# Kernel tuning notes

Hardware: AMD Instinct MI355X
Metric: run time of the kernel (lower is better)

Reference implementation:

```python
import jax, jax.numpy as jnp
import numpy as np
import math

B, C, W, H = 8, 512, 32, 32
NUM_HEADS = 4


def setup_inputs() -> dict:
    key = jax.random.key(0)
    ks = jax.random.split(key, 7)
    dqk = C // NUM_HEADS  # out channels of conv_q / conv_k
    s_in = 1.0 / math.sqrt(C)
    return {
        "x": jax.random.normal(ks[0], (B, C, W, H), dtype=jnp.float32),
        "Wq": jax.random.normal(ks[1], (dqk, C), dtype=jnp.float32) * s_in,
        "bq": jnp.zeros((dqk,), dtype=jnp.float32),
        "Wk": jax.random.normal(ks[2], (dqk, C), dtype=jnp.float32) * s_in,
        "bk": jnp.zeros((dqk,), dtype=jnp.float32),
        "Wv": jax.random.normal(ks[3], (C, C), dtype=jnp.float32) * s_in,
        "bv": jnp.zeros((C,), dtype=jnp.float32),
        "gamma": jnp.zeros((1,), dtype=jnp.float32),
    }


def reference(x, Wq, bq, Wk, bk, Wv, bv, gamma):
    b, c, w, h = x.shape
    n = w * h
    heads = NUM_HEADS
    # 1x1 convs == per-pixel linear projections
    q = jnp.einsum('bcwh,oc->bowh', x, Wq) + bq[None, :, None, None]
    k = jnp.einsum('bcwh,oc->bowh', x, Wk) + bk[None, :, None, None]
    v = jnp.einsum('bcwh,oc->bowh', x, Wv) + bv[None, :, None, None]
    # head split exactly as the torch views do
    q = q.reshape(b, heads, (c // heads) // heads, n)  # [B,H,dq,N]
    k = k.reshape(b, heads, (c // heads) // heads, n)  # [B,H,dq,N]
    v = v.reshape(b, heads, c // heads, n)             # [B,H,dv,N]
    scale = math.sqrt(c / heads)  # k_dim = in_dim / num_heads
    scores = jnp.einsum('bhdn,bhdm->bhnm', q, k) / scale  # [B,H,N,N]
    attn = jax.nn.softmax(scores, axis=-1)
    # out = v @ attn^T : out[..., c, n] = sum_m v[..., c, m] * attn[..., n, m]
    out = jnp.einsum('bhcm,bhnm->bhcn', v, attn)  # [B,H,dv,N]
    out = out.reshape(b, c, w, h)
    return gamma * out + x
```

## Files before the change

### kernel.cpp

```cpp
#include <hip/hip_runtime.h>
#include <math.h>

#define BATCH 8
#define CH    512
#define NPIX  1024
#define NH    4

typedef __attribute__((ext_vector_type(8))) short bf16x8;
typedef __attribute__((ext_vector_type(4))) float f32x4;
typedef __attribute__((ext_vector_type(16))) float f32x16;
typedef __attribute__((ext_vector_type(4))) int i32x4;
typedef __attribute__((ext_vector_type(4))) unsigned int u32x4;

#define QSC (0.088388347648318447f * 1.4426950408889634f)

#define GLOAD0(dst, addr) asm volatile("global_load_dwordx4 %0, %1, off" \
    : "=v"(dst) : "v"(addr) : "memory")
#define GLOAD1(dst, addr) asm volatile("global_load_dwordx4 %0, %1, off offset:1024" \
    : "=v"(dst) : "v"(addr) : "memory")
#define WAITV6 asm volatile("s_waitcnt vmcnt(6)" ::: "memory")
#define WAITV0 asm volatile("s_waitcnt vmcnt(0)" ::: "memory")

__device__ inline unsigned short f2bf_rne(float f) {
    unsigned int u = __float_as_uint(f);
    return (unsigned short)((u + 0x7FFFu + ((u >> 16) & 1u)) >> 16);
}
__device__ inline unsigned int pack_bf2_trunc(float a, float b) {
    return (__float_as_uint(a) >> 16) | (__float_as_uint(b) & 0xFFFF0000u);
}
__device__ inline unsigned int pack2_rne(float a, float b) {
    return (unsigned int)f2bf_rne(a) | ((unsigned int)f2bf_rne(b) << 16);
}

__global__ __launch_bounds__(256) void prep(
    const float* __restrict__ x,
    const float* __restrict__ Wq, const float* __restrict__ Wk,
    const float* __restrict__ Wv,
    unsigned short* __restrict__ XTF, unsigned short* __restrict__ WF)
{
    const int t = threadIdx.x;
    if (blockIdx.z == 8) {
        const int gid = blockIdx.y * 16 + blockIdx.x;
        #pragma unroll
        for (int rep = 0; rep < 2; ++rep) {
            const int idx = (rep * 128 + gid) * 256 + t;
            if (idx < 49152) {
                const int o = idx >> 6, k8 = idx & 63;
                const float* src;
                float sc = 1.f;
                if (o < 128)      { src = Wq + (size_t)o * CH;        sc = QSC; }
                else if (o < 256) { src = Wk + (size_t)(o - 128) * CH; }
                else              { src = Wv + (size_t)(o - 256) * CH; }
                src += k8 * 8;
                const float4 v0 = *(const float4*)src;
                const float4 v1 = *(const float4*)(src + 4);
                u32x4 st;
                st.x = pack2_rne(v0.x * sc, v0.y * sc);
                st.y = pack2_rne(v0.z * sc, v0.w * sc);
                st.z = pack2_rne(v1.x * sc, v1.y * sc);
                st.w = pack2_rne(v1.z * sc, v1.w * sc);
                const int dst = (((o >> 4) * 16 + (k8 >> 2)) * 512
                              + (((o & 15) | ((k8 & 3) << 4))) * 8);
                *(u32x4*)&WF[dst] = st;
            }
        }
        return;
    }
    __shared__ float S[64][65];
    const int a = t & 15, g = t >> 4;
    const int n0 = blockIdx.x * 64, c0 = blockIdx.y * 64, b = blockIdx.z;
    const float* xb = x + ((size_t)b * CH + c0) * NPIX + n0;
    #pragma unroll
    for (int i = 0; i < 4; ++i) {
        const int c = g + 16 * i;
        const float4 v = *(const float4*)&xb[(size_t)c * NPIX + 4 * a];
        S[c][4*a+0] = v.x; S[c][4*a+1] = v.y; S[c][4*a+2] = v.z; S[c][4*a+3] = v.w;
    }
    __syncthreads();
    const int n = t & 63;
    const int nt = (n0 >> 4) + (n >> 4);
    const int lo = n & 15;
    #pragma unroll
    for (int rep = 0; rep < 2; ++rep) {
        const int c8 = (t >> 6) + rep * 4;
        const int kkG = (c0 >> 5) + (c8 >> 2);
        const int hi = c8 & 3;
        u32x4 st;
        st.x = pack2_rne(S[c8*8+0][n], S[c8*8+1][n]);
        st.y = pack2_rne(S[c8*8+2][n], S[c8*8+3][n]);
        st.z = pack2_rne(S[c8*8+4][n], S[c8*8+5][n]);
        st.w = pack2_rne(S[c8*8+6][n], S[c8*8+7][n]);
        const size_t dst = (((size_t)b * 64 + nt) * 16 + kkG) * 512
                         + (size_t)((lo | (hi << 4))) * 8;
        *(u32x4*)&XTF[dst] = st;
    }
}

__global__ __launch_bounds__(256, 3) void qkv_proj(
    const unsigned short* __restrict__ XTF, const unsigned short* __restrict__ WF,
    const float* __restrict__ bq, const float* __restrict__ bk,
    const float* __restrict__ bv,
    unsigned short* __restrict__ QF, unsigned short* __restrict__ KF,
    unsigned short* __restrict__ VF)
{
    __shared__ unsigned short OT[4][2048];
    const int t = threadIdx.x, w = t >> 6, l = t & 63;
    const int lo = l & 15, hi = l >> 4;
    const int b = blockIdx.z;
    const int o0 = blockIdx.y * 64 + (w >> 1) * 32;
    const int n0 = blockIdx.x * 128 + (w & 1) * 64;

    const unsigned short* Ap0 = WF + (size_t)(o0 >> 4) * 8192 + l * 8;
    const unsigned short* Ap1 = Ap0 + 8192;
    const unsigned short* Bp0 = XTF + ((size_t)b * 64 + (n0 >> 4)) * 8192 + l * 8;
    const unsigned short* Bp1 = Bp0 + 8192;
    const unsigned short* Bp2 = Bp0 + 16384;
    const unsigned short* Bp3 = Bp0 + 24576;

    i32x4 ab[2][2], bb[2][4];
    GLOAD0(ab[0][0], Ap0); GLOAD0(ab[0][1], Ap1);
    GLOAD0(bb[0][0], Bp0); GLOAD0(bb[0][1], Bp1);
    GLOAD0(bb[0][2], Bp2); GLOAD0(bb[0][3], Bp3);
    Ap0 += 512; Ap1 += 512; Bp0 += 512; Bp1 += 512; Bp2 += 512; Bp3 += 512;
    GLOAD0(ab[1][0], Ap0); GLOAD0(ab[1][1], Ap1);
    GLOAD0(bb[1][0], Bp0); GLOAD0(bb[1][1], Bp1);
    GLOAD0(bb[1][2], Bp2); GLOAD0(bb[1][3], Bp3);
    Ap0 += 512; Ap1 += 512; Bp0 += 512; Bp1 += 512; Bp2 += 512; Bp3 += 512;

    f32x4 acc[2][4] = {};

    auto compute = [&](int cur) {
        bf16x8 af[2], bf[4];
        af[0] = __builtin_bit_cast(bf16x8, ab[cur][0]);
        af[1] = __builtin_bit_cast(bf16x8, ab[cur][1]);
        #pragma unroll
        for (int j = 0; j < 4; ++j) bf[j] = __builtin_bit_cast(bf16x8, bb[cur][j]);
        __builtin_amdgcn_s_setprio(1);
        #pragma unroll
        for (int i = 0; i < 2; ++i)
            #pragma unroll
            for (int j = 0; j < 4; ++j)
                acc[i][j] = __builtin_amdgcn_mfma_f32_16x16x32_bf16(af[i], bf[j], acc[i][j], 0, 0, 0);
        __builtin_amdgcn_s_setprio(0);
    };
    auto issue = [&](int cur) {
        GLOAD0(ab[cur][0], Ap0); GLOAD0(ab[cur][1], Ap1);
        GLOAD0(bb[cur][0], Bp0); GLOAD0(bb[cur][1], Bp1);
        GLOAD0(bb[cur][2], Bp2); GLOAD0(bb[cur][3], Bp3);
        Ap0 += 512; Ap1 += 512; Bp0 += 512; Bp1 += 512; Bp2 += 512; Bp3 += 512;
    };

    #pragma unroll 1
    for (int i = 0; i < 7; ++i) {
        WAITV6; __builtin_amdgcn_sched_barrier(0);
        compute(0); issue(0);
        WAITV6; __builtin_amdgcn_sched_barrier(0);
        compute(1); issue(1);
    }
    WAITV6; __builtin_amdgcn_sched_barrier(0);
    compute(0);
    WAITV0; __builtin_amdgcn_sched_barrier(0);
    compute(1);

    float bias[2][4];
    #pragma unroll
    for (int i = 0; i < 2; ++i)
        #pragma unroll
        for (int r = 0; r < 4; ++r) {
            const int orow = o0 + i * 16 + hi * 4 + r;
            if (o0 < 128)      bias[i][r] = bq[orow] * QSC;
            else if (o0 < 256) bias[i][r] = bk[orow - 128];
            else               bias[i][r] = bv[orow - 256];
        }

    if (o0 < 256) {
        const bool isQ = (o0 < 128);
        const int hh = (o0 & 127) >> 5;
        #pragma unroll
        for (int i = 0; i < 2; ++i)
            #pragma unroll
            for (int j = 0; j < 4; ++j) {
                const int nl = j * 16 + lo;
                const int og = i * 4 + hi;
                unsigned short v0 = f2bf_rne(acc[i][j][0] + bias[i][0]);
                unsigned short v1 = f2bf_rne(acc[i][j][1] + bias[i][1]);
                unsigned short v2 = f2bf_rne(acc[i][j][2] + bias[i][2]);
                unsigned short v3 = f2bf_rne(acc[i][j][3] + bias[i][3]);
                uint2 st;
                st.x = (unsigned int)v0 | ((unsigned int)v1 << 16);
                st.y = (unsigned int)v2 | ((unsigned int)v3 << 16);
                *(uint2*)&OT[w][nl * 32 + ((og ^ (nl & 7)) << 2)] = st;
            }
        unsigned short* outp = (isQ ? QF : KF) + (size_t)(b * NH + hh) * 32768;
        #pragma unroll
        for (int it = 0; it < 4; ++it) {
            const int nl = (l >> 2) + 16 * it, seg = l & 3;
            const int g0 = (2 * seg) ^ (nl & 7);
            const int g1 = (2 * seg + 1) ^ (nl & 7);
            const uint2 p0 = *(uint2*)&OT[w][nl * 32 + g0 * 4];
            const uint2 p1 = *(uint2*)&OT[w][nl * 32 + g1 * 4];
            uint4 st; st.x = p0.x; st.y = p0.y; st.z = p1.x; st.w = p1.y;
            const int nn = n0 + nl;
            const int dst = ((nn >> 5) << 10) | ((seg >> 1) << 9)
                          | ((((nn & 31) | ((seg & 1) << 5))) << 3);
            *(uint4*)&outp[dst] = st;
        }
    } else {
        const int hh  = (o0 - 256) >> 7;
        const int c64 = ((o0 - 256) >> 6) & 1;
        const int c32b= ((o0 - 256) >> 5) & 1;
        unsigned short* vfb = VF + (size_t)(b * NH + hh) * 131072
                                 + (size_t)c64 * 65536 + (size_t)c32b * 32768;
        #pragma unroll
        for (int i = 0; i < 2; ++i)
            #pragma unroll
            for (int j = 0; j < 4; ++j)
                #pragma unroll
                for (int r = 0; r < 4; ++r) {
                    const int c32 = i * 16 + hi * 4 + r;
                    const int n = n0 + j * 16 + lo;
                    const int np = (n & ~12) | ((n & 4) << 1) | ((n & 8) >> 1);
                    const int m5 = np & 31;
                    const int lidx = c32 | (((m5 >> 3) & 1) << 5);
                    const int idx = ((np >> 5) << 10) | ((m5 >> 4) << 9)
                                  | (lidx << 3) | (m5 & 7);
                    vfb[idx] = f2bf_rne(acc[i][j][r] + bias[i][r]);
                }
    }
}

__global__ __launch_bounds__(256, 4) void attn(
    const unsigned short* __restrict__ QF, const unsigned short* __restrict__ KF,
    const unsigned short* __restrict__ VF, const float* __restrict__ x,
    const float* __restrict__ gamma, float* __restrict__ out)
{
    __shared__ float Xof[4096];
    __shared__ float mlM[64], mlL[64];

    const int t = threadIdx.x, w = t >> 6, l = t & 63;
    const int xl = l & 31;
    const int h  = l >> 5;
    const int kv = w & 1, ch = w >> 1;

    const int u = blockIdx.x;
    const int xcd = u & 7;
    const int rr = u >> 3;
    const int nt = rr & 31;
    const int bh = xcd | ((rr >> 5) << 3);
    const int n0 = nt * 32;

    const unsigned short* Kp  = KF + (((size_t)bh * 32 + kv * 16) << 10) + l * 8;
    const unsigned short* Vp0 = VF + (size_t)bh * 131072 + (size_t)ch * 65536
                                   + (((size_t)kv * 16) << 10) + l * 8;
    const unsigned short* Vp1 = Vp0 + 32768;
    const unsigned short* Qa  = QF + (((size_t)bh * 32 + nt) << 10) + l * 8;

    i32x4 qr0, qr1;
    GLOAD0(qr0, Qa); GLOAD1(qr1, Qa);

    i32x4 kb[2][2], v0b[2][2], v1b[2][2];
    GLOAD0(kb[0][0], Kp);  GLOAD1(kb[0][1], Kp);
    GLOAD0(v0b[0][0], Vp0); GLOAD1(v0b[0][1], Vp0);
    GLOAD0(v1b[0][0], Vp1); GLOAD1(v1b[0][1], Vp1);
    Kp += 1024; Vp0 += 1024; Vp1 += 1024;
    GLOAD0(kb[1][0], Kp);  GLOAD1(kb[1][1], Kp);
    GLOAD0(v0b[1][0], Vp0); GLOAD1(v0b[1][1], Vp0);
    GLOAD0(v1b[1][0], Vp1); GLOAD1(v1b[1][1], Vp1);
    Kp += 1024; Vp0 += 1024; Vp1 += 1024;

    f32x16 of0 = {}; f32x16 of1 = {};
    float mrow = -INFINITY, lrow = 0.f;

    auto compute = [&](int cur) {
        const bf16x8 ck0 = __builtin_bit_cast(bf16x8, kb[cur][0]);
        const bf16x8 ck1 = __builtin_bit_cast(bf16x8, kb[cur][1]);
        const bf16x8 cv0 = __builtin_bit_cast(bf16x8, v0b[cur][0]);
        const bf16x8 cv1 = __builtin_bit_cast(bf16x8, v0b[cur][1]);
        const bf16x8 cv2 = __builtin_bit_cast(bf16x8, v1b[cur][0]);
        const bf16x8 cv3 = __builtin_bit_cast(bf16x8, v1b[cur][1]);
        const bf16x8 qf0 = __builtin_bit_cast(bf16x8, qr0);
        const bf16x8 qf1 = __builtin_bit_cast(bf16x8, qr1);

        const f32x16 z16 = {};
        __builtin_amdgcn_s_setprio(1);
        f32x16 sa = __builtin_amdgcn_mfma_f32_32x32x16_bf16(ck0, qf0, z16, 0, 0, 0);
        sa = __builtin_amdgcn_mfma_f32_32x32x16_bf16(ck1, qf1, sa, 0, 0, 0);
        __builtin_amdgcn_s_setprio(0);

        float m0x = fmaxf(fmaxf(sa[0], sa[1]), fmaxf(sa[2], sa[3]));
        float m1x = fmaxf(fmaxf(sa[4], sa[5]), fmaxf(sa[6], sa[7]));
        float m2x = fmaxf(fmaxf(sa[8], sa[9]), fmaxf(sa[10], sa[11]));
        float m3x = fmaxf(fmaxf(sa[12], sa[13]), fmaxf(sa[14], sa[15]));
        float mx = fmaxf(fmaxf(m0x, m1x), fmaxf(m2x, m3x));
        mx = fmaxf(mx, __shfl_xor(mx, 32));

        if (__any(mx > mrow + 11.5f)) {
            const float mnew = fmaxf(mrow, mx);
            const float fsc = __builtin_amdgcn_exp2f(mrow - mnew);
            mrow = mnew; lrow *= fsc;
            of0 *= fsc; of1 *= fsc;
        }

        float p[16];
        #pragma unroll
        for (int r = 0; r < 16; ++r) p[r] = __builtin_amdgcn_exp2f(sa[r] - mrow);
        lrow += (((p[0]+p[1])+(p[2]+p[3])) + ((p[4]+p[5])+(p[6]+p[7])))
              + (((p[8]+p[9])+(p[10]+p[11])) + ((p[12]+p[13])+(p[14]+p[15])));

        u32x4 w0, w1;
        w0.x = pack_bf2_trunc(p[0],  p[1]);  w0.y = pack_bf2_trunc(p[2],  p[3]);
        w0.z = pack_bf2_trunc(p[4],  p[5]);  w0.w = pack_bf2_trunc(p[6],  p[7]);
        w1.x = pack_bf2_trunc(p[8],  p[9]);  w1.y = pack_bf2_trunc(p[10], p[11]);
        w1.z = pack_bf2_trunc(p[12], p[13]); w1.w = pack_bf2_trunc(p[14], p[15]);
        const bf16x8 pf0 = __builtin_bit_cast(bf16x8, w0);
        const bf16x8 pf1 = __builtin_bit_cast(bf16x8, w1);

        __builtin_amdgcn_s_setprio(1);
        of0 = __builtin_amdgcn_mfma_f32_32x32x16_bf16(cv0, pf0, of0, 0, 0, 0);
        of0 = __builtin_amdgcn_mfma_f32_32x32x16_bf16(cv1, pf1, of0, 0, 0, 0);
        of1 = __builtin_amdgcn_mfma_f32_32x32x16_bf16(cv2, pf0, of1, 0, 0, 0);
        of1 = __builtin_amdgcn_mfma_f32_32x32x16_bf16(cv3, pf1, of1, 0, 0, 0);
        __builtin_amdgcn_s_setprio(0);
    };

    auto issue = [&](int cur) {
        GLOAD0(kb[cur][0], Kp);  GLOAD1(kb[cur][1], Kp);
        GLOAD0(v0b[cur][0], Vp0); GLOAD1(v0b[cur][1], Vp0);
        GLOAD0(v1b[cur][0], Vp1); GLOAD1(v1b[cur][1], Vp1);
        Kp += 1024; Vp0 += 1024; Vp1 += 1024;
    };

    #pragma unroll 1
    for (int i = 0; i < 7; ++i) {
        WAITV6; __builtin_amdgcn_sched_barrier(0);
        compute(0); issue(0);
        WAITV6; __builtin_amdgcn_sched_barrier(0);
        compute(1); issue(1);
    }
    WAITV6; __builtin_amdgcn_sched_barrier(0);
    compute(0);
    WAITV0; __builtin_amdgcn_sched_barrier(0);
    compute(1);

    lrow += __shfl_xor(lrow, 32);
    if (kv == 1) {
        #pragma unroll
        for (int r = 0; r < 16; ++r) {
            Xof[((ch * 2 + 0) * 16 + r) * 64 + l] = of0[r];
            Xof[((ch * 2 + 1) * 16 + r) * 64 + l] = of1[r];
        }
        if (h == 0) { mlM[ch * 32 + xl] = mrow; mlL[ch * 32 + xl] = lrow; }
    }
    __syncthreads();

    if (kv == 0) {
        const float mB = mlM[ch * 32 + xl], lB = mlL[ch * 32 + xl];
        const float ms = fmaxf(mrow, mB);
        const float fA = __builtin_amdgcn_exp2f(mrow - ms);
        const float fB = __builtin_amdgcn_exp2f(mB - ms);
        const float inv = 1.0f / (lrow * fA + lB * fB);
        const float sA = fA * inv, sB = fB * inv;
        const float g = gamma[0];
        const int b = bh >> 2, hd = bh & 3;
        const size_t base = ((size_t)b * CH + hd * 128 + ch * 64) * NPIX + n0;
        #pragma unroll
        for (int cb = 0; cb < 2; ++cb)
            #pragma unroll
            for (int r = 0; r < 16; ++r) {
                const float own = cb ? of1[r] : of0[r];
                const float dn  = Xof[((ch * 2 + cb) * 16 + r) * 64 + l];
                const int   c   = cb * 32 + (r & 3) + 8 * (r >> 2) + 4 * h;
                const size_t gi = base + (size_t)c * NPIX + xl;
                out[gi] = fmaf(g, own * sA + dn * sB, x[gi]);
            }
    }
}

extern "C" void kernel_launch(void* const* d_in, const int* in_sizes, int n_in,
                              void* d_out, int out_size, void* d_ws, size_t ws_size,
                              hipStream_t stream)
{
    const float* x     = (const float*)d_in[0];
    const float* Wq    = (const float*)d_in[1];
    const float* bq    = (const float*)d_in[2];
    const float* Wk    = (const float*)d_in[3];
    const float* bk    = (const float*)d_in[4];
    const float* Wv    = (const float*)d_in[5];
    const float* bv    = (const float*)d_in[6];
    const float* gamma = (const float*)d_in[7];
    float* out = (float*)d_out;

    char* ws = (char*)d_ws;
    unsigned short* XTFp = (unsigned short*)(ws);
    unsigned short* WFp  = (unsigned short*)(ws + 8388608);
    unsigned short* QFp  = (unsigned short*)(ws + 9175040);
    unsigned short* KFp  = (unsigned short*)(ws + 11272192);
    unsigned short* VFp  = (unsigned short*)(ws + 13369344);

    prep<<<dim3(16, 8, 9), 256, 0, stream>>>(x, Wq, Wk, Wv, XTFp, WFp);
    qkv_proj<<<dim3(8, 12, 8), 256, 0, stream>>>(XTFp, WFp, bq, bk, bv, QFp, KFp, VFp);
    attn<<<dim3(1024), 256, 0, stream>>>(QFp, KFp, VFp, x, gamma, out);
}
```

Baseline: 49.62 us.

## Process two query tiles per attention block to reuse K/V loads

Each attention block now handles 64 query pixels (two 32-wide tiles) instead of 32. Every loaded K and V fragment therefore feeds two sets of MFMAs, which halves global K/V traffic per query. The grid is halved to 512 blocks and launch bounds drop to 2 waves-per-EU hint, which doubles accumulator register use and LDS size. The trade-off is lower occupancy and fewer blocks across the CUs in exchange for more arithmetic per byte loaded.

```diff
diff --git a/kernel.cpp b/kernel.cpp
--- a/kernel.cpp
+++ b/kernel.cpp
@@ -229,13 +229,13 @@
     }
 }
 
-__global__ __launch_bounds__(256, 4) void attn(
+__global__ __launch_bounds__(256, 2) void attn(
     const unsigned short* __restrict__ QF, const unsigned short* __restrict__ KF,
     const unsigned short* __restrict__ VF, const float* __restrict__ x,
     const float* __restrict__ gamma, float* __restrict__ out)
 {
-    __shared__ float Xof[4096];
-    __shared__ float mlM[64], mlL[64];
+    __shared__ float Xof[8192];
+    __shared__ float mlM[128], mlL[128];
 
     const int t = threadIdx.x, w = t >> 6, l = t & 63;
     const int xl = l & 31;
@@ -245,18 +245,19 @@
     const int u = blockIdx.x;
     const int xcd = u & 7;
     const int rr = u >> 3;
-    const int nt = rr & 31;
-    const int bh = xcd | ((rr >> 5) << 3);
-    const int n0 = nt * 32;
+    const int nt = rr & 15;
+    const int bh = xcd | ((rr >> 4) << 3);
+    const int n0 = nt * 64;
 
     const unsigned short* Kp  = KF + (((size_t)bh * 32 + kv * 16) << 10) + l * 8;
     const unsigned short* Vp0 = VF + (size_t)bh * 131072 + (size_t)ch * 65536
                                    + (((size_t)kv * 16) << 10) + l * 8;
     const unsigned short* Vp1 = Vp0 + 32768;
-    const unsigned short* Qa  = QF + (((size_t)bh * 32 + nt) << 10) + l * 8;
-
-    i32x4 qr0, qr1;
+    const unsigned short* Qa  = QF + (((size_t)bh * 32 + nt * 2) << 10) + l * 8;
+
+    i32x4 qr0, qr1, qr2, qr3;
     GLOAD0(qr0, Qa); GLOAD1(qr1, Qa);
+    GLOAD0(qr2, Qa + 1024); GLOAD1(qr3, Qa + 1024);
 
     i32x4 kb[2][2], v0b[2][2], v1b[2][2];
     GLOAD0(kb[0][0], Kp);  GLOAD1(kb[0][1], Kp);
@@ -268,8 +269,9 @@
     GLOAD0(v1b[1][0], Vp1); GLOAD1(v1b[1][1], Vp1);
     Kp += 1024; Vp0 += 1024; Vp1 += 1024;
 
-    f32x16 of0 = {}; f32x16 of1 = {};
-    float mrow = -INFINITY, lrow = 0.f;
+    f32x16 ofA0 = {}, ofA1 = {}, ofB0 = {}, ofB1 = {};
+    float mrowA = -INFINITY, lrowA = 0.f;
+    float mrowB = -INFINITY, lrowB = 0.f;
 
     auto compute = [&](int cur) {
         const bf16x8 ck0 = __builtin_bit_cast(bf16x8, kb[cur][0]);
@@ -278,48 +280,78 @@
         const bf16x8 cv1 = __builtin_bit_cast(bf16x8, v0b[cur][1]);
         const bf16x8 cv2 = __builtin_bit_cast(bf16x8, v1b[cur][0]);
         const bf16x8 cv3 = __builtin_bit_cast(bf16x8, v1b[cur][1]);
-        const bf16x8 qf0 = __builtin_bit_cast(bf16x8, qr0);
-        const bf16x8 qf1 = __builtin_bit_cast(bf16x8, qr1);
+        const bf16x8 qA0 = __builtin_bit_cast(bf16x8, qr0);
+        const bf16x8 qA1 = __builtin_bit_cast(bf16x8, qr1);
+        const bf16x8 qB0 = __builtin_bit_cast(bf16x8, qr2);
+        const bf16x8 qB1 = __builtin_bit_cast(bf16x8, qr3);
 
         const f32x16 z16 = {};
         __builtin_amdgcn_s_setprio(1);
-        f32x16 sa = __builtin_amdgcn_mfma_f32_32x32x16_bf16(ck0, qf0, z16, 0, 0, 0);
-        sa = __builtin_amdgcn_mfma_f32_32x32x16_bf16(ck1, qf1, sa, 0, 0, 0);
+        f32x16 sa = __builtin_amdgcn_mfma_f32_32x32x16_bf16(ck0, qA0, z16, 0, 0, 0);
+        f32x16 sb = __builtin_amdgcn_mfma_f32_32x32x16_bf16(ck0, qB0, z16, 0, 0, 0);
+        sa = __builtin_amdgcn_mfma_f32_32x32x16_bf16(ck1, qA1, sa, 0, 0, 0);
+        sb = __builtin_amdgcn_mfma_f32_32x32x16_bf16(ck1, qB1, sb, 0, 0, 0);
         __builtin_amdgcn_s_setprio(0);
 
-        float m0x = fmaxf(fmaxf(sa[0], sa[1]), fmaxf(sa[2], sa[3]));
-        float m1x = fmaxf(fmaxf(sa[4], sa[5]), fmaxf(sa[6], sa[7]));
-        float m2x = fmaxf(fmaxf(sa[8], sa[9]), fmaxf(sa[10], sa[11]));
-        float m3x = fmaxf(fmaxf(sa[12], sa[13]), fmaxf(sa[14], sa[15]));
-        float mx = fmaxf(fmaxf(m0x, m1x), fmaxf(m2x, m3x));
-        mx = fmaxf(mx, __shfl_xor(mx, 32));
-
-        if (__any(mx > mrow + 11.5f)) {
-            const float mnew = fmaxf(mrow, mx);
-            const float fsc = __builtin_amdgcn_exp2f(mrow - mnew);
-            mrow = mnew; lrow *= fsc;
-            of0 *= fsc; of1 *= fsc;
-        }
-
-        float p[16];
-        #pragma unroll
-        for (int r = 0; r < 16; ++r) p[r] = __builtin_amdgcn_exp2f(sa[r] - mrow);
-        lrow += (((p[0]+p[1])+(p[2]+p[3])) + ((p[4]+p[5])+(p[6]+p[7])))
-              + (((p[8]+p[9])+(p[10]+p[11])) + ((p[12]+p[13])+(p[14]+p[15])));
-
-        u32x4 w0, w1;
-        w0.x = pack_bf2_trunc(p[0],  p[1]);  w0.y = pack_bf2_trunc(p[2],  p[3]);
-        w0.z = pack_bf2_trunc(p[4],  p[5]);  w0.w = pack_bf2_trunc(p[6],  p[7]);
-        w1.x = pack_bf2_trunc(p[8],  p[9]);  w1.y = pack_bf2_trunc(p[10], p[11]);
-        w1.z = pack_bf2_trunc(p[12], p[13]); w1.w = pack_bf2_trunc(p[14], p[15]);
-        const bf16x8 pf0 = __builtin_bit_cast(bf16x8, w0);
-        const bf16x8 pf1 = __builtin_bit_cast(bf16x8, w1);
+        float a0 = fmaxf(fmaxf(sa[0], sa[1]), fmaxf(sa[2], sa[3]));
+        float a1 = fmaxf(fmaxf(sa[4], sa[5]), fmaxf(sa[6], sa[7]));
+        float a2 = fmaxf(fmaxf(sa[8], sa[9]), fmaxf(sa[10], sa[11]));
+        float a3 = fmaxf(fmaxf(sa[12], sa[13]), fmaxf(sa[14], sa[15]));
+        float mxA = fmaxf(fmaxf(a0, a1), fmaxf(a2, a3));
+        float b0 = fmaxf(fmaxf(sb[0], sb[1]), fmaxf(sb[2], sb[3]));
+        float b1 = fmaxf(fmaxf(sb[4], sb[5]), fmaxf(sb[6], sb[7]));
+        float b2 = fmaxf(fmaxf(sb[8], sb[9]), fmaxf(sb[10], sb[11]));
+        float b3 = fmaxf(fmaxf(sb[12], sb[13]), fmaxf(sb[14], sb[15]));
+        float mxB = fmaxf(fmaxf(b0, b1), fmaxf(b2, b3));
+        mxA = fmaxf(mxA, __shfl_xor(mxA, 32));
+        mxB = fmaxf(mxB, __shfl_xor(mxB, 32));
+
+        if (__any(mxA > mrowA + 11.5f)) {
+            const float mnew = fmaxf(mrowA, mxA);
+            const float fsc = __builtin_amdgcn_exp2f(mrowA - mnew);
+            mrowA = mnew; lrowA *= fsc;
+            ofA0 *= fsc; ofA1 *= fsc;
+        }
+        if (__any(mxB > mrowB + 11.5f)) {
+            const float mnew = fmaxf(mrowB, mxB);
+            const float fsc = __builtin_amdgcn_exp2f(mrowB - mnew);
+            mrowB = mnew; lrowB *= fsc;
+            ofB0 *= fsc; ofB1 *= fsc;
+        }
+
+        float pA[16], pB[16];
+        #pragma unroll
+        for (int r = 0; r < 16; ++r) pA[r] = __builtin_amdgcn_exp2f(sa[r] - mrowA);
+        #pragma unroll
+        for (int r = 0; r < 16; ++r) pB[r] = __builtin_amdgcn_exp2f(sb[r] - mrowB);
+        lrowA += (((pA[0]+pA[1])+(pA[2]+pA[3])) + ((pA[4]+pA[5])+(pA[6]+pA[7])))
+               + (((pA[8]+pA[9])+(pA[10]+pA[11])) + ((pA[12]+pA[13])+(pA[14]+pA[15])));
+        lrowB += (((pB[0]+pB[1])+(pB[2]+pB[3])) + ((pB[4]+pB[5])+(pB[6]+pB[7])))
+               + (((pB[8]+pB[9])+(pB[10]+pB[11])) + ((pB[12]+pB[13])+(pB[14]+pB[15])));
+
+        u32x4 wA0, wA1, wB0, wB1;
+        wA0.x = pack_bf2_trunc(pA[0],  pA[1]);  wA0.y = pack_bf2_trunc(pA[2],  pA[3]);
+        wA0.z = pack_bf2_trunc(pA[4],  pA[5]);  wA0.w = pack_bf2_trunc(pA[6],  pA[7]);
+        wA1.x = pack_bf2_trunc(pA[8],  pA[9]);  wA1.y = pack_bf2_trunc(pA[10], pA[11]);
+        wA1.z = pack_bf2_trunc(pA[12], pA[13]); wA1.w = pack_bf2_trunc(pA[14], pA[15]);
+        wB0.x = pack_bf2_trunc(pB[0],  pB[1]);  wB0.y = pack_bf2_trunc(pB[2],  pB[3]);
+        wB0.z = pack_bf2_trunc(pB[4],  pB[5]);  wB0.w = pack_bf2_trunc(pB[6],  pB[7]);
+        wB1.x = pack_bf2_trunc(pB[8],  pB[9]);  wB1.y = pack_bf2_trunc(pB[10], pB[11]);
+        wB1.z = pack_bf2_trunc(pB[12], pB[13]); wB1.w = pack_bf2_trunc(pB[14], pB[15]);
+        const bf16x8 pfA0 = __builtin_bit_cast(bf16x8, wA0);
+        const bf16x8 pfA1 = __builtin_bit_cast(bf16x8, wA1);
+        const bf16x8 pfB0 = __builtin_bit_cast(bf16x8, wB0);
+        const bf16x8 pfB1 = __builtin_bit_cast(bf16x8, wB1);
 
         __builtin_amdgcn_s_setprio(1);
-        of0 = __builtin_amdgcn_mfma_f32_32x32x16_bf16(cv0, pf0, of0, 0, 0, 0);
-        of0 = __builtin_amdgcn_mfma_f32_32x32x16_bf16(cv1, pf1, of0, 0, 0, 0);
-        of1 = __builtin_amdgcn_mfma_f32_32x32x16_bf16(cv2, pf0, of1, 0, 0, 0);
-        of1 = __builtin_amdgcn_mfma_f32_32x32x16_bf16(cv3, pf1, of1, 0, 0, 0);
+        ofA0 = __builtin_amdgcn_mfma_f32_32x32x16_bf16(cv0, pfA0, ofA0, 0, 0, 0);
+        ofB0 = __builtin_amdgcn_mfma_f32_32x32x16_bf16(cv0, pfB0, ofB0, 0, 0, 0);
+        ofA0 = __builtin_amdgcn_mfma_f32_32x32x16_bf16(cv1, pfA1, ofA0, 0, 0, 0);
+        ofB0 = __builtin_amdgcn_mfma_f32_32x32x16_bf16(cv1, pfB1, ofB0, 0, 0, 0);
+        ofA1 = __builtin_amdgcn_mfma_f32_32x32x16_bf16(cv2, pfA0, ofA1, 0, 0, 0);
+        ofB1 = __builtin_amdgcn_mfma_f32_32x32x16_bf16(cv2, pfB0, ofB1, 0, 0, 0);
+        ofA1 = __builtin_amdgcn_mfma_f32_32x32x16_bf16(cv3, pfA1, ofA1, 0, 0, 0);
+        ofB1 = __builtin_amdgcn_mfma_f32_32x32x16_bf16(cv3, pfB1, ofB1, 0, 0, 0);
         __builtin_amdgcn_s_setprio(0);
     };
 
@@ -342,37 +374,63 @@
     WAITV0; __builtin_amdgcn_sched_barrier(0);
     compute(1);
 
-    lrow += __shfl_xor(lrow, 32);
+    lrowA += __shfl_xor(lrowA, 32);
+    lrowB += __shfl_xor(lrowB, 32);
     if (kv == 1) {
         #pragma unroll
         for (int r = 0; r < 16; ++r) {
-            Xof[((ch * 2 + 0) * 16 + r) * 64 + l] = of0[r];
-            Xof[((ch * 2 + 1) * 16 + r) * 64 + l] = of1[r];
-        }
-        if (h == 0) { mlM[ch * 32 + xl] = mrow; mlL[ch * 32 + xl] = lrow; }
+            Xof[((ch * 2 + 0) * 16 + r) * 64 + l]        = ofA0[r];
+            Xof[((ch * 2 + 1) * 16 + r) * 64 + l]        = ofA1[r];
+            Xof[4096 + ((ch * 2 + 0) * 16 + r) * 64 + l] = ofB0[r];
+            Xof[4096 + ((ch * 2 + 1) * 16 + r) * 64 + l] = ofB1[r];
+        }
+        if (h == 0) {
+            mlM[ch * 32 + xl] = mrowA;      mlL[ch * 32 + xl] = lrowA;
+            mlM[64 + ch * 32 + xl] = mrowB; mlL[64 + ch * 32 + xl] = lrowB;
+        }
     }
     __syncthreads();
 
     if (kv == 0) {
-        const float mB = mlM[ch * 32 + xl], lB = mlL[ch * 32 + xl];
-        const float ms = fmaxf(mrow, mB);
-        const float fA = __builtin_amdgcn_exp2f(mrow - ms);
-        const float fB = __builtin_amdgcn_exp2f(mB - ms);
-        const float inv = 1.0f / (lrow * fA + lB * fB);
-        const float sA = fA * inv, sB = fB * inv;
         const float g = gamma[0];
         const int b = bh >> 2, hd = bh & 3;
         const size_t base = ((size_t)b * CH + hd * 128 + ch * 64) * NPIX + n0;
-        #pragma unroll
-        for (int cb = 0; cb < 2; ++cb)
+        {
+            const float mB_ = mlM[ch * 32 + xl], lB_ = mlL[ch * 32 + xl];
+            const float ms = fmaxf(mrowA, mB_);
+            const float fA = __builtin_amdgcn_exp2f(mrowA - ms);
+            const float fB = __builtin_amdgcn_exp2f(mB_ - ms);
+            const float inv = 1.0f / (lrowA * fA + lB_ * fB);
+            const float sA = fA * inv, sB = fB * inv;
             #pragma unroll
-            for (int r = 0; r < 16; ++r) {
-                const float own = cb ? of1[r] : of0[r];
-                const float dn  = Xof[((ch * 2 + cb) * 16 + r) * 64 + l];
-                const int   c   = cb * 32 + (r & 3) + 8 * (r >> 2) + 4 * h;
-                const size_t gi = base + (size_t)c * NPIX + xl;
-                out[gi] = fmaf(g, own * sA + dn * sB, x[gi]);
-            }
+            for (int cb = 0; cb < 2; ++cb)
+                #pragma unroll
+                for (int r = 0; r < 16; ++r) {
+                    const float own = cb ? ofA1[r] : ofA0[r];
+                    const float dn  = Xof[((ch * 2 + cb) * 16 + r) * 64 + l];
+                    const int   c   = cb * 32 + (r & 3) + 8 * (r >> 2) + 4 * h;
+                    const size_t gi = base + (size_t)c * NPIX + xl;
+                    out[gi] = fmaf(g, own * sA + dn * sB, x[gi]);
+                }
+        }
+        {
+            const float mB_ = mlM[64 + ch * 32 + xl], lB_ = mlL[64 + ch * 32 + xl];
+            const float ms = fmaxf(mrowB, mB_);
+            const float fA = __builtin_amdgcn_exp2f(mrowB - ms);
+            const float fB = __builtin_amdgcn_exp2f(mB_ - ms);
+            const float inv = 1.0f / (lrowB * fA + lB_ * fB);
+            const float sA = fA * inv, sB = fB * inv;
+            #pragma unroll
+            for (int cb = 0; cb < 2; ++cb)
+                #pragma unroll
+                for (int r = 0; r < 16; ++r) {
+                    const float own = cb ? ofB1[r] : ofB0[r];
+                    const float dn  = Xof[4096 + ((ch * 2 + cb) * 16 + r) * 64 + l];
+                    const int   c   = cb * 32 + (r & 3) + 8 * (r >> 2) + 4 * h;
+                    const size_t gi = base + (size_t)c * NPIX + 32 + xl;
+                    out[gi] = fmaf(g, own * sA + dn * sB, x[gi]);
+                }
+        }
     }
 }
 
@@ -399,5 +457,5 @@
 
     prep<<<dim3(16, 8, 9), 256, 0, stream>>>(x, Wq, Wk, Wv, XTFp, WFp);
     qkv_proj<<<dim3(8, 12, 8), 256, 0, stream>>>(XTFp, WFp, bq, bk, bv, QFp, KFp, VFp);
-    attn<<<dim3(1024), 256, 0, stream>>>(QFp, KFp, VFp, x, gamma, out);
-}
+    attn<<<dim3(512), 256, 0, stream>>>(QFp, KFp, VFp, x, gamma, out);
+}
```

New measurement: 48.01 us. 3.2% less time.

## Deepen attention K/V prefetch to four stages and drop setprio hints

Applied to the files above, without the earlier changes.

Raises the attention kernel's register prefetch ring from two to four stages, with matching vmcnt waits, so more global loads are in flight while each step computes. Occupancy bounds are relaxed from 4 to 2 blocks per CU to make room for the extra registers. Also removes s_setprio around the MFMAs in both kernels and swaps the cross-half max shuffle for v_permlane32_swap. Lower occupancy may hurt latency hiding more than the deeper pipeline helps.

```diff
diff --git a/kernel.cpp b/kernel.cpp
--- a/kernel.cpp
+++ b/kernel.cpp
@@ -18,8 +18,11 @@
     : "=v"(dst) : "v"(addr) : "memory")
 #define GLOAD1(dst, addr) asm volatile("global_load_dwordx4 %0, %1, off offset:1024" \
     : "=v"(dst) : "v"(addr) : "memory")
-#define WAITV6 asm volatile("s_waitcnt vmcnt(6)" ::: "memory")
-#define WAITV0 asm volatile("s_waitcnt vmcnt(0)" ::: "memory")
+#define WAITV18 asm volatile("s_waitcnt vmcnt(18)" ::: "memory")
+#define WAITV12 asm volatile("s_waitcnt vmcnt(12)" ::: "memory")
+#define WAITV6  asm volatile("s_waitcnt vmcnt(6)"  ::: "memory")
+#define WAITV0  asm volatile("s_waitcnt vmcnt(0)"  ::: "memory")
+#define SB      __builtin_amdgcn_sched_barrier(0)
 
 __device__ inline unsigned short f2bf_rne(float f) {
     unsigned int u = __float_as_uint(f);
@@ -30,6 +33,11 @@
 }
 __device__ inline unsigned int pack2_rne(float a, float b) {
     return (unsigned int)f2bf_rne(a) | ((unsigned int)f2bf_rne(b) << 16);
+}
+__device__ inline float xhalf_max(float x) {
+    float a = x, b = x;
+    asm("v_permlane32_swap_b32 %0, %1" : "+v"(a), "+v"(b));
+    return fmaxf(a, b);
 }
 
 __global__ __launch_bounds__(256) void prep(
@@ -135,13 +143,11 @@
         af[1] = __builtin_bit_cast(bf16x8, ab[cur][1]);
         #pragma unroll
         for (int j = 0; j < 4; ++j) bf[j] = __builtin_bit_cast(bf16x8, bb[cur][j]);
-        __builtin_amdgcn_s_setprio(1);
         #pragma unroll
         for (int i = 0; i < 2; ++i)
             #pragma unroll
             for (int j = 0; j < 4; ++j)
                 acc[i][j] = __builtin_amdgcn_mfma_f32_16x16x32_bf16(af[i], bf[j], acc[i][j], 0, 0, 0);
-        __builtin_amdgcn_s_setprio(0);
     };
     auto issue = [&](int cur) {
         GLOAD0(ab[cur][0], Ap0); GLOAD0(ab[cur][1], Ap1);
@@ -152,14 +158,14 @@
 
     #pragma unroll 1
     for (int i = 0; i < 7; ++i) {
-        WAITV6; __builtin_amdgcn_sched_barrier(0);
+        WAITV6; SB;
         compute(0); issue(0);
-        WAITV6; __builtin_amdgcn_sched_barrier(0);
+        WAITV6; SB;
         compute(1); issue(1);
     }
-    WAITV6; __builtin_amdgcn_sched_barrier(0);
+    WAITV6; SB;
     compute(0);
-    WAITV0; __builtin_amdgcn_sched_barrier(0);
+    WAITV0; SB;
     compute(1);
 
     float bias[2][4];
@@ -229,7 +235,7 @@
     }
 }
 
-__global__ __launch_bounds__(256, 4) void attn(
+__global__ __launch_bounds__(256, 2) void attn(
     const unsigned short* __restrict__ QF, const unsigned short* __restrict__ KF,
     const unsigned short* __restrict__ VF, const float* __restrict__ x,
     const float* __restrict__ gamma, float* __restrict__ out)
@@ -258,15 +264,15 @@
     i32x4 qr0, qr1;
     GLOAD0(qr0, Qa); GLOAD1(qr1, Qa);
 
-    i32x4 kb[2][2], v0b[2][2], v1b[2][2];
-    GLOAD0(kb[0][0], Kp);  GLOAD1(kb[0][1], Kp);
-    GLOAD0(v0b[0][0], Vp0); GLOAD1(v0b[0][1], Vp0);
-    GLOAD0(v1b[0][0], Vp1); GLOAD1(v1b[0][1], Vp1);
-    Kp += 1024; Vp0 += 1024; Vp1 += 1024;
-    GLOAD0(kb[1][0], Kp);  GLOAD1(kb[1][1], Kp);
-    GLOAD0(v0b[1][0], Vp0); GLOAD1(v0b[1][1], Vp0);
-    GLOAD0(v1b[1][0], Vp1); GLOAD1(v1b[1][1], Vp1);
-    Kp += 1024; Vp0 += 1024; Vp1 += 1024;
+    i32x4 kb[4][2], v0b[4][2], v1b[4][2];
+
+    auto issue = [&](int cur) {
+        GLOAD0(kb[cur][0], Kp);   GLOAD1(kb[cur][1], Kp);
+        GLOAD0(v0b[cur][0], Vp0); GLOAD1(v0b[cur][1], Vp0);
+        GLOAD0(v1b[cur][0], Vp1); GLOAD1(v1b[cur][1], Vp1);
+        Kp += 1024; Vp0 += 1024; Vp1 += 1024;
+    };
+    issue(0); issue(1); issue(2); issue(3);
 
     f32x16 of0 = {}; f32x16 of1 = {};
     float mrow = -INFINITY, lrow = 0.f;
@@ -282,17 +288,15 @@
         const bf16x8 qf1 = __builtin_bit_cast(bf16x8, qr1);
 
         const f32x16 z16 = {};
-        __builtin_amdgcn_s_setprio(1);
         f32x16 sa = __builtin_amdgcn_mfma_f32_32x32x16_bf16(ck0, qf0, z16, 0, 0, 0);
         sa = __builtin_amdgcn_mfma_f32_32x32x16_bf16(ck1, qf1, sa, 0, 0, 0);
-        __builtin_amdgcn_s_setprio(0);
 
         float m0x = fmaxf(fmaxf(sa[0], sa[1]), fmaxf(sa[2], sa[3]));
         float m1x = fmaxf(fmaxf(sa[4], sa[5]), fmaxf(sa[6], sa[7]));
         float m2x = fmaxf(fmaxf(sa[8], sa[9]), fmaxf(sa[10], sa[11]));
         float m3x = fmaxf(fmaxf(sa[12], sa[13]), fmaxf(sa[14], sa[15]));
         float mx = fmaxf(fmaxf(m0x, m1x), fmaxf(m2x, m3x));
-        mx = fmaxf(mx, __shfl_xor(mx, 32));
+        mx = xhalf_max(mx);
 
         if (__any(mx > mrow + 11.5f)) {
             const float mnew = fmaxf(mrow, mx);
@@ -315,32 +319,23 @@
         const bf16x8 pf0 = __builtin_bit_cast(bf16x8, w0);
         const bf16x8 pf1 = __builtin_bit_cast(bf16x8, w1);
 
-        __builtin_amdgcn_s_setprio(1);
         of0 = __builtin_amdgcn_mfma_f32_32x32x16_bf16(cv0, pf0, of0, 0, 0, 0);
         of0 = __builtin_amdgcn_mfma_f32_32x32x16_bf16(cv1, pf1, of0, 0, 0, 0);
         of1 = __builtin_amdgcn_mfma_f32_32x32x16_bf16(cv2, pf0, of1, 0, 0, 0);
         of1 = __builtin_amdgcn_mfma_f32_32x32x16_bf16(cv3, pf1, of1, 0, 0, 0);
-        __builtin_amdgcn_s_setprio(0);
     };
 
-    auto issue = [&](int cur) {
-        GLOAD0(kb[cur][0], Kp);  GLOAD1(kb[cur][1], Kp);
-        GLOAD0(v0b[cur][0], Vp0); GLOAD1(v0b[cur][1], Vp0);
-        GLOAD0(v1b[cur][0], Vp1); GLOAD1(v1b[cur][1], Vp1);
-        Kp += 1024; Vp0 += 1024; Vp1 += 1024;
-    };
-
     #pragma unroll 1
-    for (int i = 0; i < 7; ++i) {
-        WAITV6; __builtin_amdgcn_sched_barrier(0);
-        compute(0); issue(0);
-        WAITV6; __builtin_amdgcn_sched_barrier(0);
-        compute(1); issue(1);
-    }
-    WAITV6; __builtin_amdgcn_sched_barrier(0);
-    compute(0);
-    WAITV0; __builtin_amdgcn_sched_barrier(0);
-    compute(1);
+    for (int i = 0; i < 3; ++i) {
+        WAITV18; SB; compute(0); issue(0);
+        WAITV18; SB; compute(1); issue(1);
+        WAITV18; SB; compute(2); issue(2);
+        WAITV18; SB; compute(3); issue(3);
+    }
+    WAITV18; SB; compute(0);
+    WAITV12; SB; compute(1);
+    WAITV6;  SB; compute(2);
+    WAITV0;  SB; compute(3);
 
     lrow += __shfl_xor(lrow, 32);
     if (kv == 1) {
```

Result: no change. 49.79 us (+0.3%).
